# Optimization experiments

Measured on AMD Instinct MI355X. Metric: run time of the kernel, lower is better.

## Reference

```python
import jax, jax.numpy as jnp
import numpy as np

NUM_EXPERTS = 16
TOP_K = 2
D_IN = 1024
D_HID = 4096
D_OUT = 1024
BATCH = 8192


def setup_inputs() -> dict:
    key = jax.random.key(0)
    ks = jax.random.split(key, 6)
    s_in = 1.0 / np.sqrt(D_IN)
    s_hid = 1.0 / np.sqrt(D_HID)
    return {
        "x": jax.random.normal(ks[0], (BATCH, D_IN), dtype=jnp.float32),
        "Wg": jax.random.normal(ks[1], (D_IN, NUM_EXPERTS), dtype=jnp.float32) * s_in,
        "W1": jax.random.normal(ks[2], (NUM_EXPERTS, D_IN, D_HID), dtype=jnp.float32) * s_in,
        "b1": jnp.zeros((NUM_EXPERTS, D_HID), dtype=jnp.float32),
        "W2": jax.random.normal(ks[3], (NUM_EXPERTS, D_HID, D_OUT), dtype=jnp.float32) * s_hid,
        "b2": jnp.zeros((NUM_EXPERTS, D_OUT), dtype=jnp.float32),
    }


def _moe_forward(x, Wg, W1, b1, W2, b2):
    # Gating: top-k routing with softmax over the selected logits.
    logits = x @ Wg                                   # [B, E]
    top_vals, top_idx = jax.lax.top_k(logits, TOP_K)  # [B, k]
    routing_weights = jax.nn.softmax(top_vals, axis=-1)  # [B, k]

    # Per-token combine weight for each expert (sum over k slots):
    # cw[b, e] = sum_k routing_weights[b, k] * (top_idx[b, k] == e)
    one_hot = jax.nn.one_hot(top_idx, NUM_EXPERTS, dtype=x.dtype)  # [B, k, E]
    combine_w = jnp.einsum("bk,bke->be", routing_weights, one_hot)  # [B, E]

    # Per-expert MLP compute + weighted scatter-add combine.
    # Fixed-size loop over experts (structurally distinct weight slices);
    # equivalent math to the original's gather/compute/scatter dispatch.
    out = jnp.zeros((x.shape[0], D_OUT), dtype=x.dtype)
    for e in range(NUM_EXPERTS):
        h = jax.nn.relu(x @ W1[e] + b1[e])            # [B, H]
        y = h @ W2[e] + b2[e]                         # [B, O]
        out = out + combine_w[:, e:e + 1] * y
    return out


def reference(x, Wg, W1, b1, W2, b2):
    return _moe_forward(x, Wg, W1, b1, W2, b2)
```

## Files before the change

### kernel.cpp

```cpp
#include <hip/hip_runtime.h>
#include <cstdio>

#define DIN   1024
#define DHID  4096
#define DOUT  1024
#define NEXP  16
#define NTOK  8192
#define NPAIR (NTOK * 2)
#define PADMAX 18432
#define MAXTILES 144

typedef _Float16 h8 __attribute__((ext_vector_type(8)));
typedef _Float16 h4 __attribute__((ext_vector_type(4)));
typedef float    f4 __attribute__((ext_vector_type(4)));

#define C_CNT  0
#define C_POFF 16
#define C_CUR  32
#define C_NT   48
#define C_TE   64
#define C_TP   256

__device__ __forceinline__ void async16(const void* g, void* l) {
  __builtin_amdgcn_global_load_lds((const __attribute__((address_space(1))) void*)g,
                                   (__attribute__((address_space(3))) void*)l, 16, 0, 0);
}

__global__ void k_init(float* __restrict__ out, const float* __restrict__ x,
                       _Float16* __restrict__ x16, int* __restrict__ ptok,
                       float* __restrict__ pw, int* __restrict__ ctrl) {
  int i = blockIdx.x * 256 + threadIdx.x;
  ((f4*)out)[i] = (f4){0.f, 0.f, 0.f, 0.f};
  float4 v = ((const float4*)x)[i];
  h4 hv = {(_Float16)v.x, (_Float16)v.y, (_Float16)v.z, (_Float16)v.w};
  ((h4*)x16)[i] = hv;
  if (i < PADMAX) { ptok[i] = 0; pw[i] = 0.f; }
  if (i < 1024) ctrl[i] = 0;
}

__global__ void k_gate(const float* __restrict__ x, const float* __restrict__ wg,
                       int* __restrict__ te, float* __restrict__ tw,
                       int* __restrict__ ctrl) {
  int t = blockIdx.x * 4 + (threadIdx.x >> 6);
  int l = threadIdx.x & 63;
  const float* xr = x + (long)t * DIN;
  float acc[NEXP];
#pragma unroll
  for (int e = 0; e < NEXP; ++e) acc[e] = 0.f;
  for (int k = l; k < DIN; k += 64) {
    float xv = xr[k];
    const float4* wr = (const float4*)(wg + (long)k * NEXP);
    float4 a = wr[0], b = wr[1], c = wr[2], d = wr[3];
    acc[0]  += xv * a.x; acc[1]  += xv * a.y; acc[2]  += xv * a.z; acc[3]  += xv * a.w;
    acc[4]  += xv * b.x; acc[5]  += xv * b.y; acc[6]  += xv * b.z; acc[7]  += xv * b.w;
    acc[8]  += xv * c.x; acc[9]  += xv * c.y; acc[10] += xv * c.z; acc[11] += xv * c.w;
    acc[12] += xv * d.x; acc[13] += xv * d.y; acc[14] += xv * d.z; acc[15] += xv * d.w;
  }
#pragma unroll
  for (int off = 32; off > 0; off >>= 1) {
#pragma unroll
    for (int e = 0; e < NEXP; ++e) acc[e] += __shfl_xor(acc[e], off, 64);
  }
  if (l == 0) {
    float v0 = -1e30f; int e0 = 0;
#pragma unroll
    for (int e = 0; e < NEXP; ++e) if (acc[e] > v0) { v0 = acc[e]; e0 = e; }
    float v1 = -1e30f; int e1 = 0;
#pragma unroll
    for (int e = 0; e < NEXP; ++e) if (e != e0 && acc[e] > v1) { v1 = acc[e]; e1 = e; }
    float d = expf(v1 - v0);
    float den = 1.f / (1.f + d);
    te[2 * t] = e0;     tw[2 * t] = den;
    te[2 * t + 1] = e1; tw[2 * t + 1] = d * den;
    atomicAdd(&ctrl[C_CNT + e0], 1);
    atomicAdd(&ctrl[C_CNT + e1], 1);
  }
}

__global__ void k_scan(int* __restrict__ ctrl) {
  __shared__ int sOff[NEXP], sT0[NEXP], sTiles[NEXP];
  int tid = threadIdx.x;
  if (tid == 0) {
    int off = 0, nt = 0;
    for (int e = 0; e < NEXP; ++e) {
      int c = ctrl[C_CNT + e];
      int tiles = (c + 127) >> 7;
      ctrl[C_POFF + e] = off;
      ctrl[C_CUR + e] = off;
      sOff[e] = off; sT0[e] = nt; sTiles[e] = tiles;
      nt += tiles;
      off += tiles * 128;
    }
    ctrl[C_NT] = nt;
  }
  __syncthreads();
  int nt = sT0[NEXP - 1] + sTiles[NEXP - 1];
  for (int j = tid; j < nt; j += blockDim.x) {
    int e = 0;
#pragma unroll
    for (int k = 1; k < NEXP; ++k) if (j >= sT0[k]) e = k;
    ctrl[C_TE + j] = e;
    ctrl[C_TP + j] = sOff[e] + (j - sT0[e]) * 128;
  }
}

__global__ void k_assign(const int* __restrict__ te, const float* __restrict__ tw,
                         int* __restrict__ ctrl, int* __restrict__ ptok,
                         float* __restrict__ pw) {
  int t = blockIdx.x * 256 + threadIdx.x;
#pragma unroll
  for (int s = 0; s < 2; ++s) {
    int e = te[2 * t + s];
    int pos = atomicAdd(&ctrl[C_CUR + e], 1);
    ptok[pos] = t;
    pw[pos] = tw[2 * t + s];
  }
}

__global__ void k_wprep(const float* __restrict__ W, _Float16* __restrict__ Wt,
                        int KD, int ND) {
  int KO = KD >> 3;
  long total = (long)NEXP * KO * ND;
  long stride = (long)gridDim.x * blockDim.x;
  for (long it = (long)blockIdx.x * blockDim.x + threadIdx.x; it < total; it += stride) {
    long n  = it & (ND - 1);
    long ko = (it / ND) & (KO - 1);
    long e  = it / ((long)ND * KO);
    const float* src = W + (e * KD + ko * 8) * ND + n;
    h8 v;
#pragma unroll
    for (int kk = 0; kk < 8; ++kk) v[kk] = (_Float16)src[(long)kk * ND];
    *(h8*)(Wt + it * 8) = v;
  }
}

template<int KD, int ND, int G1>
__global__ __launch_bounds__(256)
void k_gemm(const _Float16* __restrict__ A, const _Float16* __restrict__ Wt,
            const float* __restrict__ bias, const int* __restrict__ ctrl,
            const int* __restrict__ ptok, const float* __restrict__ pw,
            _Float16* __restrict__ Hout, float* __restrict__ out) {
  __shared__ __align__(16) _Float16 sm[32768];

  constexpr int NB = ND / 128;
  constexpr int KO = KD / 8;
  constexpr int NW = NB * MAXTILES;
  constexpr int QX = NW / 8;
  int bid = blockIdx.x;
  int wid = (bid & 7) * QX + (bid >> 3);
  int nb = wid % NB;
  int mt = wid / NB;

  if (mt >= ctrl[C_NT]) return;
  int e  = ctrl[C_TE + mt];
  int p0 = ctrl[C_TP + mt];
  int n0 = nb * 128;
  int tid = threadIdx.x;
  int w = tid >> 6, l = tid & 63;
  int wm = w & 1, wn = w >> 1;
  int ln15 = l & 15, lq = l >> 4;

  long aoff[4], boff[4];
#pragma unroll
  for (int j = 0; j < 4; ++j) {
    int r = (w * 4 + j) * 8 + (l >> 3);
    int c = (l & 7) ^ (r & 7);
    long arow = G1 ? (long)ptok[p0 + r] : (long)(p0 + r);
    aoff[j] = arow * KD + c * 8;
    boff[j] = ((long)(e * KO + c) * ND + (n0 + r)) * 8;
  }

  auto stage = [&](int t, int d) {
    _Float16* As = sm + d * 16384;
    _Float16* Bs = As + 8192;
    long ka = (long)t * 64;
    long kb = (long)t * 64 * ND;
#pragma unroll
    for (int j = 0; j < 4; ++j) {
      async16(A + aoff[j] + ka, As + (w * 4 + j) * 512);
      async16(Wt + boff[j] + kb, Bs + (w * 4 + j) * 512);
    }
  };

  f4 acc[4][4];
#pragma unroll
  for (int i = 0; i < 4; ++i)
#pragma unroll
    for (int j = 0; j < 4; ++j) acc[i][j] = (f4){0.f, 0.f, 0.f, 0.f};

  auto compute = [&](int d) {
    const _Float16* As = sm + d * 16384;
    const _Float16* Bs = As + 8192;
#pragma unroll
    for (int ks = 0; ks < 2; ++ks) {
      h8 af[4], bf[4];
      int kq = ks * 4 + lq;
#pragma unroll
      for (int i = 0; i < 4; ++i) {
        int m = wm * 64 + i * 16 + ln15;
        af[i] = *(const h8*)&As[m * 64 + (kq ^ (m & 7)) * 8];
      }
#pragma unroll
      for (int j = 0; j < 4; ++j) {
        int n = wn * 64 + j * 16 + ln15;
        bf[j] = *(const h8*)&Bs[n * 64 + (kq ^ (n & 7)) * 8];
      }
      __builtin_amdgcn_s_setprio(1);
#pragma unroll
      for (int i = 0; i < 4; ++i)
#pragma unroll
        for (int j = 0; j < 4; ++j)
          acc[i][j] = __builtin_amdgcn_mfma_f32_16x16x32_f16(af[i], bf[j], acc[i][j], 0, 0, 0);
      __builtin_amdgcn_s_setprio(0);
    }
  };

  constexpr int KSTEPS = KD / 64;

  stage(0, 0);
  __syncthreads();
#pragma unroll 1
  for (int t = 0; t < KSTEPS; t += 2) {
    stage(t + 1, 1);
    compute(0);
    __syncthreads();
    if (t + 2 < KSTEPS) stage(t + 2, 0);
    compute(1);
    __syncthreads();
  }

  float bj[4];
#pragma unroll
  for (int j = 0; j < 4; ++j) bj[j] = bias[e * ND + n0 + wn * 64 + j * 16 + ln15];

  if (G1) {
    _Float16* cs = sm;
#pragma unroll
    for (int i = 0; i < 4; ++i)
#pragma unroll
      for (int reg = 0; reg < 4; ++reg) {
        int row = wm * 64 + i * 16 + lq * 4 + reg;
#pragma unroll
        for (int j = 0; j < 4; ++j)
          cs[row * 136 + wn * 64 + j * 16 + ln15] =
              (_Float16)fmaxf(acc[i][j][reg] + bj[j], 0.f);
      }
    __syncthreads();
#pragma unroll
    for (int p = 0; p < 8; ++p) {
      int idx = p * 256 + tid;
      int row = idx >> 4, ch = idx & 15;
      *(h8*)(Hout + (long)(p0 + row) * DHID + n0 + ch * 8) =
          *(const h8*)&cs[row * 136 + ch * 8];
    }
  } else {
#pragma unroll
    for (int i = 0; i < 4; ++i)
#pragma unroll
      for (int reg = 0; reg < 4; ++reg) {
        int p = p0 + wm * 64 + i * 16 + lq * 4 + reg;
        float wgt = pw[p];
        if (wgt != 0.f) {
          int tk = ptok[p];
          float* orow = out + (long)tk * DOUT + n0 + wn * 64 + ln15;
#pragma unroll
          for (int j = 0; j < 4; ++j)
            atomicAdd(&orow[j * 16], wgt * (acc[i][j][reg] + bj[j]));
        }
      }
  }
}

extern "C" void kernel_launch(void* const* d_in, const int* in_sizes, int n_in,
                              void* d_out, int out_size, void* d_ws, size_t ws_size,
                              hipStream_t stream) {
  const float* x  = (const float*)d_in[0];
  const float* Wg = (const float*)d_in[1];
  const float* W1 = (const float*)d_in[2];
  const float* b1 = (const float*)d_in[3];
  const float* W2 = (const float*)d_in[4];
  const float* b2 = (const float*)d_in[5];
  float* out = (float*)d_out;
  char* ws = (char*)d_ws;

  size_t WT_OFF = 0;
  size_t H_OFF  = WT_OFF + (size_t)NEXP * DHID * DIN * 2;
  size_t X_OFF  = H_OFF  + (size_t)PADMAX * DHID * 2;
  size_t TE_OFF = X_OFF  + (size_t)NTOK * DIN * 2;
  size_t TW_OFF = TE_OFF + (size_t)NPAIR * 4;
  size_t PT_OFF = TW_OFF + (size_t)NPAIR * 4;
  size_t PW_OFF = PT_OFF + (size_t)PADMAX * 4;
  size_t CT_OFF = PW_OFF + (size_t)PADMAX * 4;
  size_t END    = CT_OFF + 4096;
  if (ws_size < END) {
    fprintf(stderr, "kernel_launch: ws too small (%zu < %zu)\n", ws_size, END);
    return;
  }
  _Float16* Wt  = (_Float16*)(ws + WT_OFF);
  _Float16* H   = (_Float16*)(ws + H_OFF);
  _Float16* x16 = (_Float16*)(ws + X_OFF);
  int*   te   = (int*)(ws + TE_OFF);
  float* tw   = (float*)(ws + TW_OFF);
  int*   pt   = (int*)(ws + PT_OFF);
  float* pw   = (float*)(ws + PW_OFF);
  int*   ctrl = (int*)(ws + CT_OFF);

  k_init<<<NTOK * DIN / (256 * 4), 256, 0, stream>>>(out, x, x16, pt, pw, ctrl);
  k_gate<<<NTOK / 4, 256, 0, stream>>>(x, Wg, te, tw, ctrl);
  k_scan<<<1, 256, 0, stream>>>(ctrl);
  k_assign<<<NTOK / 256, 256, 0, stream>>>(te, tw, ctrl, pt, pw);

  k_wprep<<<4096, 256, 0, stream>>>(W1, Wt, DIN, DHID);
  k_gemm<DIN, DHID, 1><<<dim3((DHID / 128) * MAXTILES), 256, 0, stream>>>(
      x16, Wt, b1, ctrl, pt, pw, H, nullptr);

  k_wprep<<<4096, 256, 0, stream>>>(W2, Wt, DHID, DOUT);
  k_gemm<DHID, DOUT, 0><<<dim3((DOUT / 128) * MAXTILES), 256, 0, stream>>>(
      H, Wt, b2, ctrl, pt, pw, nullptr, out);
}
```

Baseline: 1.345 ms.

## Single-buffer LDS in grouped GEMM to raise occupancy, split epilogue into halves

```diff
diff --git a/kernel.cpp b/kernel.cpp
--- a/kernel.cpp
+++ b/kernel.cpp
@@ -135,12 +135,12 @@
 }
 
 template<int KD, int ND, int G1>
-__global__ __launch_bounds__(256)
+__global__ __launch_bounds__(256, 5)
 void k_gemm(const _Float16* __restrict__ A, const _Float16* __restrict__ Wt,
             const float* __restrict__ bias, const int* __restrict__ ctrl,
             const int* __restrict__ ptok, const float* __restrict__ pw,
             _Float16* __restrict__ Hout, float* __restrict__ out) {
-  __shared__ __align__(16) _Float16 sm[32768];
+  __shared__ __align__(16) _Float16 sm[16384];
 
   constexpr int NB = ND / 128;
   constexpr int KO = KD / 8;
@@ -170,9 +170,9 @@
     boff[j] = ((long)(e * KO + c) * ND + (n0 + r)) * 8;
   }
 
-  auto stage = [&](int t, int d) {
-    _Float16* As = sm + d * 16384;
-    _Float16* Bs = As + 8192;
+  _Float16* As = sm;
+  _Float16* Bs = sm + 8192;
+  auto stage = [&](int t) {
     long ka = (long)t * 64;
     long kb = (long)t * 64 * ND;
 #pragma unroll
@@ -188,9 +188,7 @@
 #pragma unroll
     for (int j = 0; j < 4; ++j) acc[i][j] = (f4){0.f, 0.f, 0.f, 0.f};
 
-  auto compute = [&](int d) {
-    const _Float16* As = sm + d * 16384;
-    const _Float16* Bs = As + 8192;
+  auto compute = [&]() {
 #pragma unroll
     for (int ks = 0; ks < 2; ++ks) {
       h8 af[4], bf[4];
@@ -217,15 +215,11 @@
 
   constexpr int KSTEPS = KD / 64;
 
-  stage(0, 0);
-  __syncthreads();
 #pragma unroll 1
-  for (int t = 0; t < KSTEPS; t += 2) {
-    stage(t + 1, 1);
-    compute(0);
+  for (int t = 0; t < KSTEPS; ++t) {
+    stage(t);
     __syncthreads();
-    if (t + 2 < KSTEPS) stage(t + 2, 0);
-    compute(1);
+    compute();
     __syncthreads();
   }
 
@@ -236,22 +230,28 @@
   if (G1) {
     _Float16* cs = sm;
 #pragma unroll
-    for (int i = 0; i < 4; ++i)
-#pragma unroll
-      for (int reg = 0; reg < 4; ++reg) {
-        int row = wm * 64 + i * 16 + lq * 4 + reg;
-#pragma unroll
-        for (int j = 0; j < 4; ++j)
-          cs[row * 136 + wn * 64 + j * 16 + ln15] =
-              (_Float16)fmaxf(acc[i][j][reg] + bj[j], 0.f);
-      }
-    __syncthreads();
-#pragma unroll
-    for (int p = 0; p < 8; ++p) {
-      int idx = p * 256 + tid;
-      int row = idx >> 4, ch = idx & 15;
-      *(h8*)(Hout + (long)(p0 + row) * DHID + n0 + ch * 8) =
-          *(const h8*)&cs[row * 136 + ch * 8];
+    for (int h = 0; h < 2; ++h) {
+      if (wn == h) {
+#pragma unroll
+        for (int i = 0; i < 4; ++i)
+#pragma unroll
+          for (int reg = 0; reg < 4; ++reg) {
+            int row = wm * 64 + i * 16 + lq * 4 + reg;
+#pragma unroll
+            for (int j = 0; j < 4; ++j)
+              cs[row * 68 + j * 16 + ln15] =
+                  (_Float16)fmaxf(acc[i][j][reg] + bj[j], 0.f);
+          }
+      }
+      __syncthreads();
+#pragma unroll
+      for (int p = 0; p < 4; ++p) {
+        int idx = p * 256 + tid;
+        int row = idx >> 3, ch = idx & 7;
+        *(h8*)(Hout + (long)(p0 + row) * DHID + n0 + h * 64 + ch * 8) =
+            *(const h8*)&cs[row * 68 + ch * 8];
+      }
+      if (h == 0) __syncthreads();
     }
   } else {
 #pragma unroll
```

New measurement: 2.453 ms. 1.82x slower.
